# Kernel tuning notes

Measured on AMD Instinct MI355X. Metric: run time of the kernel, lower is better.

## Reference

```python
import jax, jax.numpy as jnp
import numpy as np

N_NODES, N_EDGES = 50000, 800000
D_H, D_E, HID = 128, 64, 128  # dim_in = D_H + D_E = 192; hidden_dim2 = D_H + HID = 256


def setup_inputs() -> dict:
    key = jax.random.key(0)
    k1, k2, k3, k4, k5 = jax.random.split(key, 5)
    H = jax.random.normal(k1, (N_NODES, D_H), dtype=jnp.float32)
    idx = jax.random.randint(k2, (2, N_EDGES), 0, N_NODES)
    X_e = jax.random.normal(k3, (N_EDGES, D_E), dtype=jnp.float32)
    # kaiming_normal (fan_in mode, relu gain): std = sqrt(2 / fan_in)
    W1 = jax.random.normal(k4, (D_H + D_E, HID), dtype=jnp.float32) * np.sqrt(2.0 / (D_H + D_E)).astype(np.float32)
    W2 = jax.random.normal(k5, (D_H + HID, HID), dtype=jnp.float32) * np.sqrt(2.0 / (D_H + HID)).astype(np.float32)
    return {"H": H, "idx": idx, "X_e": X_e, "W1": W1, "W2": W2}


def reference(H, idx, X_e, W1, W2):
    # gather source-node embeddings and concat with edge features: [E, d_h + d_e]
    x = jnp.concatenate([H[idx[0]], X_e], axis=1)
    y = jax.nn.relu(x @ W1)                                   # [E, HID]
    # scatter_max into destination nodes; empty segments -> 0 (torch_scatter zero fill).
    y = jax.ops.segment_max(y, idx[1], num_segments=H.shape[0])
    y = jnp.maximum(y, 0.0)  # relu output >= 0, so this only fixes -inf empties
    y = jnp.concatenate([H, y], axis=1)                       # [N, d_h + HID]
    y = jax.nn.relu(y @ W2)                                   # [N, HID]
    return y + H  # residual connection (HID == d_h)
```

## Files before the change

### kernel.cpp

```cpp
#include <hip/hip_runtime.h>
#include <hip/hip_bf16.h>
#include <stdint.h>

#define N_NODES 50000
#define N_EDGES 800000
#define D_H 128
#define D_E 64
#define HID 128

#define MTILE 96
#define SMAX 16
#define N_ETILES ((N_EDGES + MTILE - 1) / MTILE)

#define SCAN_B 512
#define N_CHUNKS ((N_NODES + SCAN_B - 1) / SCAN_B)

typedef __attribute__((ext_vector_type(8))) short bf16x8;
typedef __attribute__((ext_vector_type(4))) short s16x4;
typedef __attribute__((ext_vector_type(4))) float f32x4;
typedef __attribute__((ext_vector_type(4))) int i32x4;

__device__ __forceinline__ unsigned short f2bf(float x) {
    unsigned int u = __float_as_uint(x);
    u += 0x7FFFu + ((u >> 16) & 1u);
    return (unsigned short)(u >> 16);
}

__device__ __forceinline__ s16x4 pack4(const f32x4 v) {
    s16x4 o = { (short)f2bf(v[0]), (short)f2bf(v[1]),
                (short)f2bf(v[2]), (short)f2bf(v[3]) };
    return o;
}

__device__ __forceinline__ bf16x8 pack8(const f32x4 a, const f32x4 b) {
    bf16x8 o = { (short)f2bf(a[0]), (short)f2bf(a[1]), (short)f2bf(a[2]), (short)f2bf(a[3]),
                 (short)f2bf(b[0]), (short)f2bf(b[1]), (short)f2bf(b[2]), (short)f2bf(b[3]) };
    return o;
}

#define NG4 (N_NODES * HID / 4)
#define ND4 (N_NODES / 4)
#define NHB4 (N_NODES * D_H / 4)
#define NW1 (192 * HID)
#define NW2 (256 * HID)
#define ZB  ((NG4 + ND4 + 255) / 256)
#define CB  ((NHB4 + NW1 + NW2 + 255) / 256)
__global__ void prep0(const float* __restrict__ H,
                      const float* __restrict__ W1,
                      const float* __restrict__ W2,
                      float* __restrict__ gmax, int* __restrict__ deg,
                      unsigned short* __restrict__ Hb,
                      unsigned short* __restrict__ W1t,
                      unsigned short* __restrict__ W2t) {
    const int b = blockIdx.x;
    if (b < ZB) {
        const int i = b * 256 + threadIdx.x;
        if (i < NG4) {
            ((f32x4*)gmax)[i] = f32x4{0.f, 0.f, 0.f, 0.f};
        } else if (i < NG4 + ND4) {
            ((i32x4*)deg)[i - NG4] = i32x4{0, 0, 0, 0};
        }
    } else {
        const int i = (b - ZB) * 256 + threadIdx.x;
        if (i < NHB4) {
            ((s16x4*)Hb)[i] = pack4(((const f32x4*)H)[i]);
        } else if (i < NHB4 + NW1) {
            const int j = i - NHB4;
            const int n = j / 192, k = j - n * 192;
            W1t[j] = f2bf(W1[k * HID + n]);
        } else if (i < NHB4 + NW1 + NW2) {
            const int j = i - NHB4 - NW1;
            const int n = j >> 8, k = j & 255;
            W2t[j] = f2bf(W2[k * HID + n]);
        }
    }
}

__global__ void hist(const int* __restrict__ idx, int* __restrict__ deg) {
    const int i = blockIdx.x * blockDim.x + threadIdx.x;
    if (i < N_EDGES / 4) {
        const i32x4 d4 = ((const i32x4*)(idx + N_EDGES))[i];
        atomicAdd(&deg[d4.x], 1);
        atomicAdd(&deg[d4.y], 1);
        atomicAdd(&deg[d4.z], 1);
        atomicAdd(&deg[d4.w], 1);
    }
}

__global__ void scan_a(const int* __restrict__ deg, int* __restrict__ sc,
                       int* __restrict__ totals) {
    __shared__ int s[SCAN_B];
    const int tid = threadIdx.x;
    const int i = blockIdx.x * SCAN_B + tid;
    const int v = (i < N_NODES) ? deg[i] : 0;
    s[tid] = v;
    __syncthreads();
    for (int o = 1; o < SCAN_B; o <<= 1) {
        int t = (tid >= o) ? s[tid - o] : 0;
        __syncthreads();
        s[tid] += t;
        __syncthreads();
    }
    if (i < N_NODES) sc[i] = s[tid] - v;
    if (tid == SCAN_B - 1) totals[blockIdx.x] = s[SCAN_B - 1];
}

__global__ void scan_b(int* __restrict__ totals) {
    __shared__ int s[128];
    const int tid = threadIdx.x;
    const int v = (tid < N_CHUNKS) ? totals[tid] : 0;
    s[tid] = v;
    __syncthreads();
    for (int o = 1; o < 128; o <<= 1) {
        int t = (tid >= o) ? s[tid - o] : 0;
        __syncthreads();
        s[tid] += t;
        __syncthreads();
    }
    if (tid < N_CHUNKS) totals[tid] = s[tid] - v;
}

__global__ void scan_c(const int* __restrict__ sc, const int* __restrict__ totals,
                       int* __restrict__ cursor) {
    const int i = blockIdx.x * SCAN_B + threadIdx.x;
    if (i < N_NODES) cursor[i] = sc[i] + totals[blockIdx.x];
}

__global__ void scatter(const int* __restrict__ idx, int* __restrict__ cursor,
                        unsigned long long* __restrict__ pk8) {
    const int i = blockIdx.x * blockDim.x + threadIdx.x;
    if (i < N_EDGES / 4) {
        const i32x4 s4 = ((const i32x4*)idx)[i];
        const i32x4 d4 = ((const i32x4*)(idx + N_EDGES))[i];
        #pragma unroll
        for (int q = 0; q < 4; ++q) {
            const int e = i * 4 + q;
            const int s = (q == 0) ? s4.x : (q == 1) ? s4.y : (q == 2) ? s4.z : s4.w;
            const int d = (q == 0) ? d4.x : (q == 1) ? d4.y : (q == 2) ? d4.z : d4.w;
            const int p = atomicAdd(&cursor[d], 1);
            pk8[p] = (unsigned long long)(unsigned)e |
                     ((unsigned long long)(unsigned)s << 20) |
                     ((unsigned long long)(unsigned)d << 37);
        }
    }
}

__global__ __launch_bounds__(256, 3)
void edge_sorted(const float* __restrict__ H,
                 const unsigned short* __restrict__ Hb,
                 const float* __restrict__ Xe,
                 const float* __restrict__ W1,
                 const unsigned short* __restrict__ W1t,
                 const unsigned long long* __restrict__ pk8,
                 float* __restrict__ gmax, int useAux) {
    __shared__ unsigned short sX[MTILE][200];
    __shared__ float ymax[SMAX + 1][132];
    __shared__ int rowD[MTILE];
    __shared__ int segNode[SMAX];
    __shared__ int sWaveTot[4];
    __shared__ unsigned char rowG[MTILE];

    const int tid  = threadIdx.x;
    const int wave = tid >> 6;
    const int lane = tid & 63;
    const int p0   = blockIdx.x * MTILE;

    const int col = lane & 15;
    const int kr0 = (lane >> 4) * 8;

    if (useAux) {
        #pragma unroll
        for (int it = 0; it < 6; ++it) {
            const int j   = tid + it * 256;
            const int row = j >> 4;
            const int c8  = (j & 15) * 8;
            int pe = p0 + row; if (pe >= N_EDGES) pe = N_EDGES - 1;
            const int src = (int)((pk8[pe] >> 20) & 0x1FFFFull);
            *(bf16x8*)&sX[row][c8] = *(const bf16x8*)(Hb + (size_t)src * D_H + c8);
        }
    } else {
        #pragma unroll
        for (int it = 0; it < 12; ++it) {
            const int j   = tid + it * 256;
            const int row = j >> 5;
            const int c4  = (j & 31) * 4;
            int pe = p0 + row; if (pe >= N_EDGES) pe = N_EDGES - 1;
            const int src = (int)((pk8[pe] >> 20) & 0x1FFFFull);
            const f32x4 v = *(const f32x4*)(H + (size_t)src * D_H + c4);
            *(s16x4*)&sX[row][c4] = pack4(v);
        }
    }
    #pragma unroll
    for (int it = 0; it < 3; ++it) {
        const int j   = tid + it * 256;
        const int row = j >> 3;
        const int c8  = (j & 7) * 8;
        int pe = p0 + row; if (pe >= N_EDGES) pe = N_EDGES - 1;
        const int e = (int)(pk8[pe] & 0xFFFFFull);
        const float* p = Xe + (size_t)e * D_E + c8;
        *(bf16x8*)&sX[row][128 + c8] = pack8(*(const f32x4*)p, *(const f32x4*)(p + 4));
    }

    bf16x8 bfrag[6][2];
    if (useAux) {
        #pragma unroll
        for (int ks = 0; ks < 6; ++ks)
            #pragma unroll
            for (int nf = 0; nf < 2; ++nf) {
                const int n = wave * 32 + nf * 16 + col;
                bfrag[ks][nf] = *(const bf16x8*)&W1t[(size_t)n * 192 + ks * 32 + kr0];
            }
    } else {
        #pragma unroll
        for (int ks = 0; ks < 6; ++ks)
            #pragma unroll
            for (int nf = 0; nf < 2; ++nf) {
                const int n  = wave * 32 + nf * 16 + col;
                const int kb = ks * 32 + kr0;
                bf16x8 b;
                #pragma unroll
                for (int f = 0; f < 8; ++f) b[f] = (short)f2bf(W1[(kb + f) * HID + n]);
                bfrag[ks][nf] = b;
            }
    }

    const int pe0 = p0 + tid;
    const bool inTile = (tid < MTILE);
    const bool valid  = inTile && (pe0 < N_EDGES);
    int d = 0;
    if (inTile) {
        const int pc = valid ? pe0 : (N_EDGES - 1);
        d = (int)(pk8[pc] >> 37);
        rowD[tid] = d;
    }
    int dp = __shfl_up(d, 1);
    if (lane == 0 && inTile && tid > 0) dp = (int)(pk8[pe0 - 1] >> 37);
    const bool flag = valid && (tid == 0 || d != dp);
    const unsigned long long m = __ballot(flag);
    if (lane == 0) sWaveTot[wave] = (int)__popcll(m);

    for (int i2 = tid; i2 < (SMAX + 1) * 132; i2 += 256) ((float*)ymax)[i2] = 0.f;
    __syncthreads();

    int g = 255;
    if (valid) {
        const unsigned long long le =
            (lane == 63) ? ~0ull : ((1ull << (lane + 1)) - 1);
        g = (int)__popcll(m & le) - 1 + ((wave == 1) ? sWaveTot[0] : 0);
    }
    if (inTile) rowG[tid] = (unsigned char)(valid ? g : 255);
    if (flag && g < SMAX) segNode[g] = d;
    __syncthreads();

    f32x4 acc[6][2];
    #pragma unroll
    for (int mm = 0; mm < 6; ++mm) {
        acc[mm][0] = f32x4{0.f, 0.f, 0.f, 0.f};
        acc[mm][1] = f32x4{0.f, 0.f, 0.f, 0.f};
    }
    const int arow = lane & 15;
    __builtin_amdgcn_s_setprio(1);
    #pragma unroll
    for (int ks = 0; ks < 6; ++ks)
        #pragma unroll
        for (int mm = 0; mm < 6; ++mm) {
            bf16x8 a = *(const bf16x8*)&sX[mm * 16 + arow][ks * 32 + kr0];
            acc[mm][0] = __builtin_amdgcn_mfma_f32_16x16x32_bf16(a, bfrag[ks][0], acc[mm][0], 0, 0, 0);
            acc[mm][1] = __builtin_amdgcn_mfma_f32_16x16x32_bf16(a, bfrag[ks][1], acc[mm][1], 0, 0, 0);
        }
    __builtin_amdgcn_s_setprio(0);

    const int rb = (lane >> 4) * 4;
    const int cb = wave * 32 + col;
    #pragma unroll
    for (int mm = 0; mm < 6; ++mm) {
        const int r0 = mm * 16 + rb;
        const int g0 = rowG[r0];
        const int g3 = rowG[r0 + 3];
        if (g0 == g3) {
            const float v0 = fmaxf(fmaxf(acc[mm][0][0], acc[mm][0][1]),
                                   fmaxf(acc[mm][0][2], acc[mm][0][3]));
            const float v1 = fmaxf(fmaxf(acc[mm][1][0], acc[mm][1][1]),
                                   fmaxf(acc[mm][1][2], acc[mm][1][3]));
            if (g0 < SMAX) {
                if (v0 > 0.f) atomicMax((int*)&ymax[g0][cb],      __float_as_int(v0));
                if (v1 > 0.f) atomicMax((int*)&ymax[g0][cb + 16], __float_as_int(v1));
            } else if (g0 < 255) {
                float* base = gmax + (size_t)rowD[r0] * HID;
                if (v0 > 0.f) atomicMax((int*)(base + cb),      __float_as_int(v0));
                if (v1 > 0.f) atomicMax((int*)(base + cb + 16), __float_as_int(v1));
            }
        } else {
            #pragma unroll
            for (int r = 0; r < 4; ++r) {
                const int gg = rowG[r0 + r];
                const float v0 = acc[mm][0][r];
                const float v1 = acc[mm][1][r];
                if (gg < SMAX) {
                    if (v0 > 0.f) atomicMax((int*)&ymax[gg][cb],      __float_as_int(v0));
                    if (v1 > 0.f) atomicMax((int*)&ymax[gg][cb + 16], __float_as_int(v1));
                } else if (gg < 255) {
                    float* base = gmax + (size_t)rowD[r0 + r] * HID;
                    if (v0 > 0.f) atomicMax((int*)(base + cb),      __float_as_int(v0));
                    if (v1 > 0.f) atomicMax((int*)(base + cb + 16), __float_as_int(v1));
                }
            }
        }
    }
    __syncthreads();

    const int nSeg = sWaveTot[0] + sWaveTot[1];
    const int nS = (nSeg < SMAX) ? nSeg : SMAX;
    for (int i2 = tid; i2 < nS * 128; i2 += 256) {
        const int sg = i2 >> 7;
        const int c  = i2 & 127;
        const float v = ymax[sg][c];
        float* dst = gmax + (size_t)segNode[sg] * HID + c;
        if (sg == 0 || sg == nSeg - 1) {
            if (v > 0.f) atomicMax((int*)dst, __float_as_int(v));
        } else {
            *dst = v;
        }
    }
}

__global__ __launch_bounds__(256, 4)
void node_mlp(const float* __restrict__ H,
              const float* __restrict__ gmax,
              const float* __restrict__ W2,
              const unsigned short* __restrict__ W2t,
              float* __restrict__ out, int useAux) {
    __shared__ unsigned short sA[64][264];

    const int tid  = threadIdx.x;
    const int wave = tid >> 6;
    const int lane = tid & 63;
    const int base = blockIdx.x * 64;

    const int col = lane & 15;
    const int kr0 = (lane >> 4) * 8;
    bf16x8 bfrag[8][2];
    if (useAux) {
        #pragma unroll
        for (int ks = 0; ks < 8; ++ks)
            #pragma unroll
            for (int nf = 0; nf < 2; ++nf) {
                const int n = wave * 32 + nf * 16 + col;
                bfrag[ks][nf] = *(const bf16x8*)&W2t[(size_t)n * 256 + ks * 32 + kr0];
            }
    } else {
        #pragma unroll
        for (int ks = 0; ks < 8; ++ks)
            #pragma unroll
            for (int nf = 0; nf < 2; ++nf) {
                const int n  = wave * 32 + nf * 16 + col;
                const int kb = ks * 32 + kr0;
                bf16x8 b;
                #pragma unroll
                for (int f = 0; f < 8; ++f) b[f] = (short)f2bf(W2[(kb + f) * HID + n]);
                bfrag[ks][nf] = b;
            }
    }

    #pragma unroll
    for (int it = 0; it < 8; ++it) {
        const int i   = tid + it * 256;
        const int row = i >> 5;
        const int c4  = (i & 31) * 4;
        int node = base + row;
        if (node >= N_NODES) node = N_NODES - 1;
        *(s16x4*)&sA[row][c4] = pack4(*(const f32x4*)(H + (size_t)node * D_H + c4));
    }
    #pragma unroll
    for (int it = 0; it < 8; ++it) {
        const int i   = tid + it * 256;
        const int row = i >> 5;
        const int c4  = (i & 31) * 4;
        int node = base + row;
        if (node >= N_NODES) node = N_NODES - 1;
        *(s16x4*)&sA[row][128 + c4] = pack4(*(const f32x4*)(gmax + (size_t)node * HID + c4));
    }
    __syncthreads();

    f32x4 acc[4][2];
    #pragma unroll
    for (int mm = 0; mm < 4; ++mm) {
        acc[mm][0] = f32x4{0.f, 0.f, 0.f, 0.f};
        acc[mm][1] = f32x4{0.f, 0.f, 0.f, 0.f};
    }
    const int arow = lane & 15;
    __builtin_amdgcn_s_setprio(1);
    #pragma unroll
    for (int ks = 0; ks < 8; ++ks)
        #pragma unroll
        for (int mm = 0; mm < 4; ++mm) {
            bf16x8 a = *(const bf16x8*)&sA[mm * 16 + arow][ks * 32 + kr0];
            acc[mm][0] = __builtin_amdgcn_mfma_f32_16x16x32_bf16(a, bfrag[ks][0], acc[mm][0], 0, 0, 0);
            acc[mm][1] = __builtin_amdgcn_mfma_f32_16x16x32_bf16(a, bfrag[ks][1], acc[mm][1], 0, 0, 0);
        }
    __builtin_amdgcn_s_setprio(0);

    const int rb = (lane >> 4) * 4;
    #pragma unroll
    for (int mm = 0; mm < 4; ++mm)
        #pragma unroll
        for (int r = 0; r < 4; ++r) {
            const int node = base + mm * 16 + rb + r;
            if (node < N_NODES) {
                const size_t o = (size_t)node * HID + wave * 32 + col;
                out[o]      = fmaxf(acc[mm][0][r], 0.f) + H[o];
                out[o + 16] = fmaxf(acc[mm][1][r], 0.f) + H[o + 16];
            }
        }
}

extern "C" void kernel_launch(void* const* d_in, const int* in_sizes, int n_in,
                              void* d_out, int out_size, void* d_ws, size_t ws_size,
                              hipStream_t stream) {
    const float* H   = (const float*)d_in[0];
    const int*   idx = (const int*)d_in[1];
    const float* Xe  = (const float*)d_in[2];
    const float* W1  = (const float*)d_in[3];
    const float* W2  = (const float*)d_in[4];
    float* out = (float*)d_out;

    char* ws = (char*)d_ws;
    float* gmax   = (float*)(ws);
    int*   deg    = (int*)(ws + 25600000);
    int*   sc     = (int*)(ws + 25800192);
    int*   totals = (int*)(ws + 26000384);
    unsigned long long* pk8 = (unsigned long long*)(ws + 26000896);
    unsigned short* W1t = (unsigned short*)(ws + 32400896);
    unsigned short* W2t = (unsigned short*)(ws + 32450048);
    unsigned short* Hb  = (unsigned short*)(ws + 32515584);
    const int useAux = (ws_size >= (size_t)45315584) ? 1 : 0;

    const int nPrep = ZB + (useAux ? CB : 0);
    prep0<<<nPrep, 256, 0, stream>>>(H, W1, W2, gmax, deg, Hb, W1t, W2t);
    hist<<<(N_EDGES / 4 + 255) / 256, 256, 0, stream>>>(idx, deg);
    scan_a<<<N_CHUNKS, SCAN_B, 0, stream>>>(deg, sc, totals);
    scan_b<<<1, 128, 0, stream>>>(totals);
    scan_c<<<N_CHUNKS, SCAN_B, 0, stream>>>(sc, totals, deg);
    scatter<<<(N_EDGES / 4 + 255) / 256, 256, 0, stream>>>(idx, deg, pk8);
    edge_sorted<<<N_ETILES, 256, 0, stream>>>(H, Hb, Xe, W1, W1t, pk8, gmax, useAux);
    node_mlp<<<(N_NODES + 63) / 64, 256, 0, stream>>>(H, gmax, W2, W2t, out, useAux);
}
```

Measured before the change: 250.9 us.

## Pre-permute edge features into sorted order as bf16 during scatter

The scatter kernel now processes one edge per thread and, when the workspace is large enough, reads each block's 256 edge-feature rows contiguously, converts them to bf16, and writes them to their destination-sorted position in a new buffer. The edge kernel then reads these sorted bf16 rows contiguously instead of gathering fp32 rows by edge id. This replaces a random fp32 gather with a coalesced read plus a scattered bf16 write of half the size. It also drops the 4-edge vectorized index load and needs a much larger workspace, so the new path only runs if the harness provides that space.

```diff
diff --git a/kernel.cpp b/kernel.cpp
--- a/kernel.cpp
+++ b/kernel.cpp
@@ -127,20 +127,30 @@
 }
 
 __global__ void scatter(const int* __restrict__ idx, int* __restrict__ cursor,
-                        unsigned long long* __restrict__ pk8) {
-    const int i = blockIdx.x * blockDim.x + threadIdx.x;
-    if (i < N_EDGES / 4) {
-        const i32x4 s4 = ((const i32x4*)idx)[i];
-        const i32x4 d4 = ((const i32x4*)(idx + N_EDGES))[i];
-        #pragma unroll
-        for (int q = 0; q < 4; ++q) {
-            const int e = i * 4 + q;
-            const int s = (q == 0) ? s4.x : (q == 1) ? s4.y : (q == 2) ? s4.z : s4.w;
-            const int d = (q == 0) ? d4.x : (q == 1) ? d4.y : (q == 2) ? d4.z : d4.w;
-            const int p = atomicAdd(&cursor[d], 1);
-            pk8[p] = (unsigned long long)(unsigned)e |
-                     ((unsigned long long)(unsigned)s << 20) |
-                     ((unsigned long long)(unsigned)d << 37);
+                        unsigned long long* __restrict__ pk8,
+                        const float* __restrict__ Xe,
+                        unsigned short* __restrict__ Xeb, int useXeb) {
+    __shared__ int sp[256];
+    const int tid = threadIdx.x;
+    const int i = blockIdx.x * 256 + tid;
+    const int s = idx[i];
+    const int d = idx[N_EDGES + i];
+    const int p = atomicAdd(&cursor[d], 1);
+    pk8[p] = (unsigned long long)(unsigned)i |
+             ((unsigned long long)(unsigned)s << 20) |
+             ((unsigned long long)(unsigned)d << 37);
+    if (useXeb) {
+        sp[tid] = p;
+        __syncthreads();
+        const int base = blockIdx.x * 256;
+        #pragma unroll
+        for (int it = 0; it < 8; ++it) {
+            const int j   = tid + it * 256;
+            const int row = j >> 3;
+            const int c8  = (j & 7) * 8;
+            const float* ps = Xe + (size_t)(base + row) * D_E + c8;
+            *(bf16x8*)(Xeb + (size_t)sp[row] * D_E + c8) =
+                pack8(*(const f32x4*)ps, *(const f32x4*)(ps + 4));
         }
     }
 }
@@ -149,10 +159,11 @@
 void edge_sorted(const float* __restrict__ H,
                  const unsigned short* __restrict__ Hb,
                  const float* __restrict__ Xe,
+                 const unsigned short* __restrict__ Xeb,
                  const float* __restrict__ W1,
                  const unsigned short* __restrict__ W1t,
                  const unsigned long long* __restrict__ pk8,
-                 float* __restrict__ gmax, int useAux) {
+                 float* __restrict__ gmax, int useAux, int useXeb) {
     __shared__ unsigned short sX[MTILE][200];
     __shared__ float ymax[SMAX + 1][132];
     __shared__ int rowD[MTILE];
@@ -190,15 +201,26 @@
             *(s16x4*)&sX[row][c4] = pack4(v);
         }
     }
-    #pragma unroll
-    for (int it = 0; it < 3; ++it) {
-        const int j   = tid + it * 256;
-        const int row = j >> 3;
-        const int c8  = (j & 7) * 8;
-        int pe = p0 + row; if (pe >= N_EDGES) pe = N_EDGES - 1;
-        const int e = (int)(pk8[pe] & 0xFFFFFull);
-        const float* p = Xe + (size_t)e * D_E + c8;
-        *(bf16x8*)&sX[row][128 + c8] = pack8(*(const f32x4*)p, *(const f32x4*)(p + 4));
+    if (useXeb) {
+        #pragma unroll
+        for (int it = 0; it < 3; ++it) {
+            const int j   = tid + it * 256;
+            const int row = j >> 3;
+            const int c8  = (j & 7) * 8;
+            int pe = p0 + row; if (pe >= N_EDGES) pe = N_EDGES - 1;
+            *(bf16x8*)&sX[row][128 + c8] = *(const bf16x8*)(Xeb + (size_t)pe * D_E + c8);
+        }
+    } else {
+        #pragma unroll
+        for (int it = 0; it < 3; ++it) {
+            const int j   = tid + it * 256;
+            const int row = j >> 3;
+            const int c8  = (j & 7) * 8;
+            int pe = p0 + row; if (pe >= N_EDGES) pe = N_EDGES - 1;
+            const int e = (int)(pk8[pe] & 0xFFFFFull);
+            const float* p = Xe + (size_t)e * D_E + c8;
+            *(bf16x8*)&sX[row][128 + c8] = pack8(*(const f32x4*)p, *(const f32x4*)(p + 4));
+        }
     }
 
     bf16x8 bfrag[6][2];
@@ -433,7 +455,9 @@
     unsigned short* W1t = (unsigned short*)(ws + 32400896);
     unsigned short* W2t = (unsigned short*)(ws + 32450048);
     unsigned short* Hb  = (unsigned short*)(ws + 32515584);
+    unsigned short* Xeb = (unsigned short*)(ws + 45315584);
     const int useAux = (ws_size >= (size_t)45315584) ? 1 : 0;
+    const int useXeb = (ws_size >= (size_t)147715584) ? 1 : 0;
 
     const int nPrep = ZB + (useAux ? CB : 0);
     prep0<<<nPrep, 256, 0, stream>>>(H, W1, W2, gmax, deg, Hb, W1t, W2t);
@@ -441,7 +465,8 @@
     scan_a<<<N_CHUNKS, SCAN_B, 0, stream>>>(deg, sc, totals);
     scan_b<<<1, 128, 0, stream>>>(totals);
     scan_c<<<N_CHUNKS, SCAN_B, 0, stream>>>(sc, totals, deg);
-    scatter<<<(N_EDGES / 4 + 255) / 256, 256, 0, stream>>>(idx, deg, pk8);
-    edge_sorted<<<N_ETILES, 256, 0, stream>>>(H, Hb, Xe, W1, W1t, pk8, gmax, useAux);
+    scatter<<<N_EDGES / 256, 256, 0, stream>>>(idx, deg, pk8, Xe, Xeb, useXeb);
+    edge_sorted<<<N_ETILES, 256, 0, stream>>>(H, Hb, Xe, Xeb, W1, W1t, pk8,
+                                              gmax, useAux, useXeb);
     node_mlp<<<(N_NODES + 63) / 64, 256, 0, stream>>>(H, gmax, W2, W2t, out, useAux);
 }
```

Result: slower. 272.7 us (+8.7%).
